# Kernel tuning notes

Hardware: AMD Instinct MI355X
Metric: run time of the kernel (lower is better)

Reference implementation:

```python
import jax, jax.numpy as jnp
import numpy as np

D_MODEL = 1024
D_HEAD = 128
B, S = 4, 4096


def apply_rope(x, cos, sin):
    # x: [B,S,d_head], cos/sin: [S, d_head//2]
    half = x.shape[-1] // 2
    x1, x2 = x[..., :half], x[..., half:]
    cos = cos[None, :, :].astype(x.dtype)
    sin = sin[None, :, :].astype(x.dtype)
    return jnp.concatenate([x1 * cos - x2 * sin, x1 * sin + x2 * cos], axis=-1)


def setup_inputs() -> dict:
    key = jax.random.key(0)
    ks = jax.random.split(key, 10)
    x = jax.random.normal(ks[0], (B, S, D_MODEL), dtype=jnp.float32)
    # realistic RoPE tables
    half = D_HEAD // 2
    inv_freq = 1.0 / (10000.0 ** (np.arange(0, half, dtype=np.float32) / half))
    pos = np.arange(S, dtype=np.float32)
    ang = pos[:, None] * inv_freq[None, :]
    cos = jnp.asarray(np.cos(ang), dtype=jnp.float32)
    sin = jnp.asarray(np.sin(ang), dtype=jnp.float32)
    # True where key index > query index (masked positions)
    causal_mask = jnp.triu(jnp.ones((S, S), dtype=bool), k=1)
    scale_w = 1.0 / np.sqrt(D_MODEL)
    Wq1 = jax.random.normal(ks[1], (D_MODEL, D_HEAD), dtype=jnp.float32) * scale_w
    Wq2 = jax.random.normal(ks[2], (D_MODEL, D_HEAD), dtype=jnp.float32) * scale_w
    Wk1 = jax.random.normal(ks[3], (D_MODEL, D_HEAD), dtype=jnp.float32) * scale_w
    Wk2 = jax.random.normal(ks[4], (D_MODEL, D_HEAD), dtype=jnp.float32) * scale_w
    Wv = jax.random.normal(ks[5], (D_MODEL, D_HEAD), dtype=jnp.float32) * scale_w
    Wo = jax.random.normal(ks[6], (D_HEAD, D_MODEL), dtype=jnp.float32) * (1.0 / np.sqrt(D_HEAD))
    return {"x": x, "cos": cos, "sin": sin, "causal_mask": causal_mask,
            "Wq1": Wq1, "Wq2": Wq2, "Wk1": Wk1, "Wk2": Wk2, "Wv": Wv, "Wo": Wo}


def reference(x, cos, sin, causal_mask, Wq1, Wq2, Wk1, Wk2, Wv, Wo):
    q1 = apply_rope(jnp.einsum('bsD,Dd->bsd', x, Wq1), cos, sin)
    q2 = apply_rope(jnp.einsum('bsD,Dd->bsd', x, Wq2), cos, sin)
    k1 = apply_rope(jnp.einsum('bsD,Dd->bsd', x, Wk1), cos, sin)
    k2 = apply_rope(jnp.einsum('bsD,Dd->bsd', x, Wk2), cos, sin)
    v = jnp.einsum('bsD,Dd->bsd', x, Wv)
    scale = 1.0 / np.sqrt(D_HEAD)
    a1 = jnp.einsum('bsd,btd->bst', q1, k1) * scale
    a2 = jnp.einsum('bsd,btd->bst', q2, k2) * scale
    a = jnp.where(causal_mask[None, :, :], 0.0, a1 * a2)
    out = jnp.einsum('bst,btd->bsd', a, v)
    return jnp.einsum('bsd,dD->bsD', out, Wo)
```

## Files before the change

kernel.cpp:

```cpp
#include <hip/hip_runtime.h>
#include <stdint.h>
#include <stddef.h>

typedef _Float16 f16;
typedef __attribute__((ext_vector_type(8))) _Float16 f16x8;
typedef __attribute__((ext_vector_type(4))) _Float16 f16x4;
typedef __attribute__((ext_vector_type(16))) float f32x16;
typedef __attribute__((ext_vector_type(8))) float f32x8v;
typedef __attribute__((ext_vector_type(4))) float floatx4;

#define MFMA(a, b, c) __builtin_amdgcn_mfma_f32_32x32x16_f16((a), (b), (c), 0, 0, 0)

typedef const __attribute__((address_space(1))) void gvoid_t;
typedef __attribute__((address_space(3))) void svoid_t;

__device__ __forceinline__ void gload_lds16(const void* g, void* l) {
  __builtin_amdgcn_global_load_lds((gvoid_t*)g, (svoid_t*)l, 16, 0, 0);
}

__global__ __launch_bounds__(256) void k_transpose_cvt(const float* __restrict__ W,
                                                       f16* __restrict__ Wt, int K, int N) {
  __shared__ float t[32][33];
  int k0 = blockIdx.x * 32, n0 = blockIdx.y * 32;
  int tx = threadIdx.x & 31, ty = threadIdx.x >> 5;
#pragma unroll
  for (int i = 0; i < 4; ++i)
    t[ty + 8 * i][tx] = W[(size_t)(k0 + ty + 8 * i) * N + n0 + tx];
  __syncthreads();
#pragma unroll
  for (int i = 0; i < 4; ++i)
    Wt[(size_t)(n0 + ty + 8 * i) * K + k0 + tx] = (f16)t[tx][ty + 8 * i];
}

__global__ __launch_bounds__(256, 2) void k_proj(const float* __restrict__ X,
                                                 const f16* __restrict__ Bt,
                                                 const float* __restrict__ cosp,
                                                 const float* __restrict__ sinp,
                                                 f16* __restrict__ q1h, f16* __restrict__ q2h,
                                                 f16* __restrict__ k1h, f16* __restrict__ k2h,
                                                 f16* __restrict__ vh) {
  __shared__ __align__(16) float Af[128 * 64];
  __shared__ __align__(16) f16 Bs[128 * 64];
  int tid = threadIdx.x;
  int wave = tid >> 6, lane = tid & 63;
  int m0 = blockIdx.y * 128, n0 = blockIdx.x;
  int wm = wave * 32;
  int rl = lane & 31, h = lane >> 5;
  int srow = lane >> 3, sslot = lane & 7;
  int arow = lane >> 4, aslot = lane & 15;
  const f16* Bmat = Bt + (size_t)n0 * 128 * 1024;

  f32x16 acc[4];
#pragma unroll
  for (int nb = 0; nb < 4; ++nb)
#pragma unroll
    for (int r = 0; r < 16; ++r) acc[nb][r] = 0.f;

  for (int k0 = 0; k0 < 1024; k0 += 64) {
    __syncthreads();
#pragma unroll
    for (int c = 0; c < 8; ++c) {
      int chunk = c * 4 + wave;
      int r = chunk * 4 + arow;
      int src16 = (((aslot >> 1) ^ (r & 7)) << 1) | (aslot & 1);
      gload_lds16(X + (size_t)(m0 + r) * 1024 + k0 + src16 * 4, Af + chunk * 256);
    }
#pragma unroll
    for (int c = 0; c < 4; ++c) {
      int chunk = c * 4 + wave;
      int r = chunk * 8 + srow;
      int cb = sslot ^ (r & 7);
      gload_lds16(Bmat + (size_t)r * 1024 + k0 + cb * 8, Bs + chunk * 512);
    }
    __syncthreads();

#pragma unroll
    for (int kb = 0; kb < 4; ++kb) {
      int s = 2 * kb + h;
      int ra = wm + rl;
      f32x8v a8 = *(const f32x8v*)(Af + ra * 64 + ((s ^ (ra & 7)) * 8));
      f16x8 af;
#pragma unroll
      for (int e = 0; e < 8; ++e) af[e] = (f16)a8[e];
      f16x8 bf[4];
#pragma unroll
      for (int nb = 0; nb < 4; ++nb) {
        int rb = nb * 32 + rl;
        bf[nb] = *(const f16x8*)(Bs + rb * 64 + (s ^ (rb & 7)) * 8);
      }
#pragma unroll
      for (int nb = 0; nb < 4; ++nb) acc[nb] = MFMA(af, bf[nb], acc[nb]);
    }
  }

  if (n0 == 4) {
#pragma unroll
    for (int r = 0; r < 16; ++r) {
      int irow = (r & 3) + 8 * (r >> 2) + 4 * h;
      int gr = m0 + wm + irow;
#pragma unroll
      for (int nb = 0; nb < 4; ++nb)
        vh[(size_t)gr * 128 + nb * 32 + rl] = (f16)acc[nb][r];
    }
  } else {
    f16* outp = (n0 == 0) ? q1h : (n0 == 1) ? q2h : (n0 == 2) ? k1h : k2h;
#pragma unroll
    for (int r = 0; r < 16; ++r) {
      int irow = (r & 3) + 8 * (r >> 2) + 4 * h;
      int gr = m0 + wm + irow;
      int s = gr & 4095;
#pragma unroll
      for (int nb = 0; nb < 2; ++nb) {
        int d = nb * 32 + rl;
        float c = cosp[s * 64 + d], sn = sinp[s * 64 + d];
        float a = acc[nb][r], bb = acc[nb + 2][r];
        outp[(size_t)gr * 128 + d]      = (f16)(a * c - bb * sn);
        outp[(size_t)gr * 128 + 64 + d] = (f16)(a * sn + bb * c);
      }
    }
  }
}

__global__ __launch_bounds__(256) void k_vtrans16(const f16* __restrict__ vh,
                                                  f16* __restrict__ vt) {
  __shared__ unsigned short t[32][33];
  int r0 = blockIdx.x * 32, d0 = blockIdx.y * 32;
  int tx = threadIdx.x & 31, ty = threadIdx.x >> 5;
#pragma unroll
  for (int i = 0; i < 4; ++i)
    t[ty + 8 * i][tx] = ((const unsigned short*)vh)[(size_t)(r0 + ty + 8 * i) * 128 + d0 + tx];
  __syncthreads();
  int b = r0 >> 12, s0 = r0 & 4095;
#pragma unroll
  for (int i = 0; i < 4; ++i)
    ((unsigned short*)vt)[((size_t)(b * 128 + d0 + ty + 8 * i)) * 4096 + s0 + tx] =
        t[tx][ty + 8 * i];
}

__global__ __launch_bounds__(256, 2) void k_s(const f16* __restrict__ q1h,
                                              const f16* __restrict__ q2h,
                                              const f16* __restrict__ k1h,
                                              const f16* __restrict__ k2h,
                                              f16* __restrict__ P) {
  __shared__ __align__(16) f16 A1[128 * 64];
  __shared__ __align__(16) f16 A2[128 * 64];
  __shared__ __align__(16) f16 B1[128 * 64];
  __shared__ __align__(16) f16 B2[128 * 64];
  int bid0 = blockIdx.x;
  int bid = (bid0 & 7) * 264 + (bid0 >> 3);
  int b = bid / 528, t = bid % 528;
  int i = (int)((sqrtf(8.f * t + 1.f) - 1.f) * 0.5f);
  if ((i + 1) * (i + 2) / 2 <= t) ++i;
  if (i * (i + 1) / 2 > t) --i;
  int j = t - i * (i + 1) / 2;

  int tid = threadIdx.x;
  int wave = tid >> 6, lane = tid & 63;
  int wm = (wave >> 1) * 64, wn = (wave & 1) * 64;
  int rl = lane & 31, h = lane >> 5;
  int srow = lane >> 3, sslot = lane & 7;
  size_t rowA = (size_t)b * 4096 + i * 128;
  size_t rowB = (size_t)b * 4096 + j * 128;

  f32x16 acc1[2][2], acc2[2][2];
#pragma unroll
  for (int mb = 0; mb < 2; ++mb)
#pragma unroll
    for (int nb = 0; nb < 2; ++nb)
#pragma unroll
      for (int r = 0; r < 16; ++r) { acc1[mb][nb][r] = 0.f; acc2[mb][nb][r] = 0.f; }

  for (int k0 = 0; k0 < 128; k0 += 64) {
    __syncthreads();
#pragma unroll
    for (int c = 0; c < 4; ++c) {
      int chunk = c * 4 + wave;
      int r = chunk * 8 + srow;
      int cb = sslot ^ (r & 7);
      gload_lds16(q1h + (rowA + r) * 128 + k0 + cb * 8, A1 + chunk * 512);
      gload_lds16(q2h + (rowA + r) * 128 + k0 + cb * 8, A2 + chunk * 512);
      gload_lds16(k1h + (rowB + r) * 128 + k0 + cb * 8, B1 + chunk * 512);
      gload_lds16(k2h + (rowB + r) * 128 + k0 + cb * 8, B2 + chunk * 512);
    }
    __syncthreads();

#pragma unroll
    for (int kb = 0; kb < 4; ++kb) {
      int s = 2 * kb + h;
      f16x8 a1f[2], a2f[2], b1f[2], b2f[2];
#pragma unroll
      for (int mb = 0; mb < 2; ++mb) {
        int r = wm + mb * 32 + rl;
        int off = r * 64 + (s ^ (r & 7)) * 8;
        a1f[mb] = *(const f16x8*)(A1 + off);
        a2f[mb] = *(const f16x8*)(A2 + off);
      }
#pragma unroll
      for (int nb = 0; nb < 2; ++nb) {
        int r = wn + nb * 32 + rl;
        int off = r * 64 + (s ^ (r & 7)) * 8;
        b1f[nb] = *(const f16x8*)(B1 + off);
        b2f[nb] = *(const f16x8*)(B2 + off);
      }
#pragma unroll
      for (int mb = 0; mb < 2; ++mb)
#pragma unroll
        for (int nb = 0; nb < 2; ++nb) {
          acc1[mb][nb] = MFMA(a1f[mb], b1f[nb], acc1[mb][nb]);
          acc2[mb][nb] = MFMA(a2f[mb], b2f[nb], acc2[mb][nb]);
        }
    }
  }

  f16* pt = P + ((size_t)b * 528 + t) * 16384;
  bool diag = (i == j);
#pragma unroll
  for (int mb = 0; mb < 2; ++mb)
#pragma unroll
    for (int nb = 0; nb < 2; ++nb)
#pragma unroll
      for (int r = 0; r < 16; ++r) {
        int row_l = wm + mb * 32 + (r & 3) + 8 * (r >> 2) + 4 * h;
        int col_l = wn + nb * 32 + rl;
        float p = acc1[mb][nb][r] * acc2[mb][nb][r] * (1.0f / 128.0f);
        if (diag && col_l > row_l) p = 0.f;
        pt[(size_t)row_l * 128 + col_l] = (f16)p;
      }
}

__global__ __launch_bounds__(256, 2) void k_pv(const f16* __restrict__ P,
                                               const f16* __restrict__ vt,
                                               f16* __restrict__ o0, f16* __restrict__ o1,
                                               f16* __restrict__ o2, f16* __restrict__ o3) {
  __shared__ __align__(16) f16 As[128 * 64];
  __shared__ __align__(16) f16 Bs[128 * 64];
  int bid = blockIdx.x;
  int b = bid / 80, c = bid % 80;
  int qt, s;
  if (c < 8)       { qt = c;                 s = 0; }
  else if (c < 24) { int t = c - 8;  qt = 8  + (t >> 1); s = t & 1; }
  else if (c < 48) { int t = c - 24; qt = 16 + t / 3;    s = t - 3 * (t / 3); }
  else             { int t = c - 48; qt = 24 + (t >> 2); s = t & 3; }
  int tq = qt * (qt + 1) / 2;
  const f16* Pb = P + (size_t)b * 528 * 16384;
  const f16* vb = vt + (size_t)b * 128 * 4096;
  int kbase = s * 1024;
  int kend = (qt + 1) * 128 < kbase + 1024 ? (qt + 1) * 128 : kbase + 1024;

  int tid = threadIdx.x;
  int wave = tid >> 6, lane = tid & 63;
  int wm = (wave >> 1) * 64, wn = (wave & 1) * 64;
  int rl = lane & 31, h = lane >> 5;
  int srow = lane >> 3, sslot = lane & 7;

  f32x16 acc[2][2];
#pragma unroll
  for (int mb = 0; mb < 2; ++mb)
#pragma unroll
    for (int nb = 0; nb < 2; ++nb)
#pragma unroll
      for (int r = 0; r < 16; ++r) acc[mb][nb][r] = 0.f;

  for (int k0 = kbase; k0 < kend; k0 += 64) {
    int jt = k0 >> 7, koff = k0 & 127;
    const f16* Pt = Pb + (size_t)(tq + jt) * 16384;
    __syncthreads();
#pragma unroll
    for (int c4 = 0; c4 < 4; ++c4) {
      int chunk = c4 * 4 + wave;
      int r = chunk * 8 + srow;
      int cb = sslot ^ (r & 7);
      gload_lds16(Pt + (size_t)r * 128 + koff + cb * 8, As + chunk * 512);
      gload_lds16(vb + (size_t)r * 4096 + k0 + cb * 8, Bs + chunk * 512);
    }
    __syncthreads();

#pragma unroll
    for (int kb = 0; kb < 4; ++kb) {
      int sidx = 2 * kb + h;
      f16x8 af[2], bf[2];
#pragma unroll
      for (int mb = 0; mb < 2; ++mb) {
        int r = wm + mb * 32 + rl;
        af[mb] = *(const f16x8*)(As + r * 64 + (sidx ^ (r & 7)) * 8);
      }
#pragma unroll
      for (int nb = 0; nb < 2; ++nb) {
        int r = wn + nb * 32 + rl;
        bf[nb] = *(const f16x8*)(Bs + r * 64 + (sidx ^ (r & 7)) * 8);
      }
#pragma unroll
      for (int mb = 0; mb < 2; ++mb)
#pragma unroll
        for (int nb = 0; nb < 2; ++nb)
          acc[mb][nb] = MFMA(af[mb], bf[nb], acc[mb][nb]);
    }
  }

  f16* op = (s == 0) ? o0 : (s == 1) ? o1 : (s == 2) ? o2 : o3;
#pragma unroll
  for (int mb = 0; mb < 2; ++mb)
#pragma unroll
    for (int nb = 0; nb < 2; ++nb)
#pragma unroll
      for (int r = 0; r < 16; ++r) {
        int gr = b * 4096 + qt * 128 + wm + mb * 32 + (r & 3) + 8 * (r >> 2) + 4 * h;
        op[(size_t)gr * 128 + wn + nb * 32 + rl] = (f16)acc[mb][nb][r];
      }
}

__global__ __launch_bounds__(256, 2) void k_gout(const f16* __restrict__ o0,
                                                 const f16* __restrict__ o1,
                                                 const f16* __restrict__ o2,
                                                 const f16* __restrict__ o3,
                                                 const f16* __restrict__ Bt,
                                                 float* __restrict__ C) {
  __shared__ __align__(16) f16 As[128 * 64];
  __shared__ __align__(16) f16 Bs[128 * 64];
  int tid = threadIdx.x;
  int wave = tid >> 6, lane = tid & 63;
  int m0 = blockIdx.y * 128, n0 = blockIdx.x * 128;
  int wm = (wave >> 1) * 64, wn = (wave & 1) * 64;
  int rl = lane & 31, h = lane >> 5;
  int srow = lane >> 3, sslot = lane & 7;
  int qt = (m0 >> 7) & 31;
  int ns = (qt >> 3) + 1;
  const f16* srcs[4] = {o0, o1, o2, o3};

  f32x16 acc[2][2];
#pragma unroll
  for (int mb = 0; mb < 2; ++mb)
#pragma unroll
    for (int nb = 0; nb < 2; ++nb)
#pragma unroll
      for (int r = 0; r < 16; ++r) acc[mb][nb][r] = 0.f;

  for (int k0 = 0; k0 < 128; k0 += 64) {
    __syncthreads();
#pragma unroll
    for (int c = 0; c < 4; ++c) {
      int chunk = c * 4 + wave;
      int r = chunk * 8 + srow;
      float sum[8];
#pragma unroll
      for (int e = 0; e < 8; ++e) sum[e] = 0.f;
#pragma unroll
      for (int p = 0; p < 4; ++p) {
        if (p < ns) {
          f16x8 v = *(const f16x8*)(srcs[p] + (size_t)(m0 + r) * 128 + k0 + sslot * 8);
#pragma unroll
          for (int e = 0; e < 8; ++e) sum[e] += (float)v[e];
        }
      }
      f16x8 w;
#pragma unroll
      for (int e = 0; e < 8; ++e) w[e] = (f16)sum[e];
      *(f16x8*)(As + r * 64 + (sslot ^ (r & 7)) * 8) = w;
      int cb = sslot ^ (r & 7);
      gload_lds16(Bt + (size_t)(n0 + r) * 128 + k0 + cb * 8, Bs + chunk * 512);
    }
    __syncthreads();

#pragma unroll
    for (int kb = 0; kb < 4; ++kb) {
      int s = 2 * kb + h;
      f16x8 af[2], bf[2];
#pragma unroll
      for (int mb = 0; mb < 2; ++mb) {
        int r = wm + mb * 32 + rl;
        af[mb] = *(const f16x8*)(As + r * 64 + (s ^ (r & 7)) * 8);
      }
#pragma unroll
      for (int nb = 0; nb < 2; ++nb) {
        int r = wn + nb * 32 + rl;
        bf[nb] = *(const f16x8*)(Bs + r * 64 + (s ^ (r & 7)) * 8);
      }
#pragma unroll
      for (int mb = 0; mb < 2; ++mb)
#pragma unroll
        for (int nb = 0; nb < 2; ++nb)
          acc[mb][nb] = MFMA(af[mb], bf[nb], acc[mb][nb]);
    }
  }

#pragma unroll
  for (int mb = 0; mb < 2; ++mb)
#pragma unroll
    for (int nb = 0; nb < 2; ++nb)
#pragma unroll
      for (int r = 0; r < 16; ++r) {
        int i = m0 + wm + mb * 32 + (r & 3) + 8 * (r >> 2) + 4 * h;
        int j = n0 + wn + nb * 32 + rl;
        C[(size_t)i * 1024 + j] = acc[mb][nb][r];
      }
}

extern "C" void kernel_launch(void* const* d_in, const int* in_sizes, int n_in,
                              void* d_out, int out_size, void* d_ws, size_t ws_size,
                              hipStream_t stream) {
  (void)in_sizes; (void)n_in; (void)out_size; (void)ws_size;
  const float* x  = (const float*)d_in[0];
  const float* cp = (const float*)d_in[1];
  const float* sp = (const float*)d_in[2];
  const float* W[5] = {(const float*)d_in[4], (const float*)d_in[5], (const float*)d_in[6],
                       (const float*)d_in[7], (const float*)d_in[8]};
  const float* Wo = (const float*)d_in[9];
  float* out = (float*)d_out;
  char* ws = (char*)d_ws;

  const size_t OFF_H    = 33554432;
  const size_t OFF_WTH  = OFF_H + 6 * 4194304;
  const size_t OFF_WOTH = OFF_WTH + 1310720;
  const size_t OFF_P    = OFF_WOTH + 262144;
  f16*   o0   = (f16*)(ws + 0);
  f16*   o1   = (f16*)(ws + 4194304);
  f16*   o2   = (f16*)(ws + 8388608);
  f16*   o3   = (f16*)(ws + 12582912);
  f16*   q1h  = (f16*)(ws + OFF_H + 0 * 4194304);
  f16*   q2h  = (f16*)(ws + OFF_H + 1 * 4194304);
  f16*   k1h  = (f16*)(ws + OFF_H + 2 * 4194304);
  f16*   k2h  = (f16*)(ws + OFF_H + 3 * 4194304);
  f16*   vh   = (f16*)(ws + OFF_H + 4 * 4194304);
  f16*   vt   = (f16*)(ws + OFF_H + 5 * 4194304);
  f16*   Wth  = (f16*)(ws + OFF_WTH);
  f16*   Woth = (f16*)(ws + OFF_WOTH);
  f16*   P    = (f16*)(ws + OFF_P);

  for (int w = 0; w < 5; ++w)
    k_transpose_cvt<<<dim3(32, 4), 256, 0, stream>>>(W[w], Wth + (size_t)w * 128 * 1024, 1024, 128);
  k_transpose_cvt<<<dim3(4, 32), 256, 0, stream>>>(Wo, Woth, 128, 1024);
  k_proj<<<dim3(5, 128), 256, 0, stream>>>(x, Wth, cp, sp, q1h, q2h, k1h, k2h, vh);
  k_vtrans16<<<dim3(512, 4), 256, 0, stream>>>(vh, vt);
  k_s<<<2112, 256, 0, stream>>>(q1h, q2h, k1h, k2h, P);
  k_pv<<<320, 256, 0, stream>>>(P, vt, o0, o1, o2, o3);
  k_gout<<<dim3(8, 128), 256, 0, stream>>>(o0, o1, o2, o3, Woth, out);
}
```

Measured before the change: 163.5 us.

## Pre-convert X to fp16 and remap projection block order for L2 locality

Result: faster. 151.4 us (-7.4%).

```diff
diff --git a/kernel.cpp b/kernel.cpp
--- a/kernel.cpp
+++ b/kernel.cpp
@@ -6,7 +6,6 @@
 typedef __attribute__((ext_vector_type(8))) _Float16 f16x8;
 typedef __attribute__((ext_vector_type(4))) _Float16 f16x4;
 typedef __attribute__((ext_vector_type(16))) float f32x16;
-typedef __attribute__((ext_vector_type(8))) float f32x8v;
 typedef __attribute__((ext_vector_type(4))) float floatx4;
 
 #define MFMA(a, b, c) __builtin_amdgcn_mfma_f32_32x32x16_f16((a), (b), (c), 0, 0, 0)
@@ -16,6 +15,17 @@
 
 __device__ __forceinline__ void gload_lds16(const void* g, void* l) {
   __builtin_amdgcn_global_load_lds((gvoid_t*)g, (svoid_t*)l, 16, 0, 0);
+}
+
+__global__ __launch_bounds__(256) void k_cvt_f16(const float* __restrict__ in,
+                                                 f16* __restrict__ out, int n4) {
+  int i = blockIdx.x * 256 + threadIdx.x;
+  if (i < n4) {
+    floatx4 v = ((const floatx4*)in)[i];
+    f16x4 o;
+    o[0] = (f16)v[0]; o[1] = (f16)v[1]; o[2] = (f16)v[2]; o[3] = (f16)v[3];
+    ((f16x4*)out)[i] = o;
+  }
 }
 
 __global__ __launch_bounds__(256) void k_transpose_cvt(const float* __restrict__ W,
@@ -32,22 +42,24 @@
     Wt[(size_t)(n0 + ty + 8 * i) * K + k0 + tx] = (f16)t[tx][ty + 8 * i];
 }
 
-__global__ __launch_bounds__(256, 2) void k_proj(const float* __restrict__ X,
+__global__ __launch_bounds__(256, 2) void k_proj(const f16* __restrict__ A,
                                                  const f16* __restrict__ Bt,
                                                  const float* __restrict__ cosp,
                                                  const float* __restrict__ sinp,
                                                  f16* __restrict__ q1h, f16* __restrict__ q2h,
                                                  f16* __restrict__ k1h, f16* __restrict__ k2h,
                                                  f16* __restrict__ vh) {
-  __shared__ __align__(16) float Af[128 * 64];
+  __shared__ __align__(16) f16 As[128 * 64];
   __shared__ __align__(16) f16 Bs[128 * 64];
+  int bid = blockIdx.x;
+  int c8 = bid & 7, t = bid >> 3;
+  int n0 = t % 5;
+  int m0 = (c8 + 8 * (t / 5)) * 128;
   int tid = threadIdx.x;
   int wave = tid >> 6, lane = tid & 63;
-  int m0 = blockIdx.y * 128, n0 = blockIdx.x;
   int wm = wave * 32;
   int rl = lane & 31, h = lane >> 5;
   int srow = lane >> 3, sslot = lane & 7;
-  int arow = lane >> 4, aslot = lane & 15;
   const f16* Bmat = Bt + (size_t)n0 * 128 * 1024;
 
   f32x16 acc[4];
@@ -58,18 +70,12 @@
 
   for (int k0 = 0; k0 < 1024; k0 += 64) {
     __syncthreads();
-#pragma unroll
-    for (int c = 0; c < 8; ++c) {
-      int chunk = c * 4 + wave;
-      int r = chunk * 4 + arow;
-      int src16 = (((aslot >> 1) ^ (r & 7)) << 1) | (aslot & 1);
-      gload_lds16(X + (size_t)(m0 + r) * 1024 + k0 + src16 * 4, Af + chunk * 256);
-    }
 #pragma unroll
     for (int c = 0; c < 4; ++c) {
       int chunk = c * 4 + wave;
       int r = chunk * 8 + srow;
       int cb = sslot ^ (r & 7);
+      gload_lds16(A + (size_t)(m0 + r) * 1024 + k0 + cb * 8, As + chunk * 512);
       gload_lds16(Bmat + (size_t)r * 1024 + k0 + cb * 8, Bs + chunk * 512);
     }
     __syncthreads();
@@ -78,10 +84,7 @@
     for (int kb = 0; kb < 4; ++kb) {
       int s = 2 * kb + h;
       int ra = wm + rl;
-      f32x8v a8 = *(const f32x8v*)(Af + ra * 64 + ((s ^ (ra & 7)) * 8));
-      f16x8 af;
-#pragma unroll
-      for (int e = 0; e < 8; ++e) af[e] = (f16)a8[e];
+      f16x8 af = *(const f16x8*)(As + ra * 64 + (s ^ (ra & 7)) * 8);
       f16x8 bf[4];
 #pragma unroll
       for (int nb = 0; nb < 4; ++nb) {
@@ -408,7 +411,8 @@
   float* out = (float*)d_out;
   char* ws = (char*)d_ws;
 
-  const size_t OFF_H    = 33554432;
+  const size_t OFF_XH   = 16777216;
+  const size_t OFF_H    = OFF_XH + 33554432;
   const size_t OFF_WTH  = OFF_H + 6 * 4194304;
   const size_t OFF_WOTH = OFF_WTH + 1310720;
   const size_t OFF_P    = OFF_WOTH + 262144;
@@ -416,6 +420,7 @@
   f16*   o1   = (f16*)(ws + 4194304);
   f16*   o2   = (f16*)(ws + 8388608);
   f16*   o3   = (f16*)(ws + 12582912);
+  f16*   xh   = (f16*)(ws + OFF_XH);
   f16*   q1h  = (f16*)(ws + OFF_H + 0 * 4194304);
   f16*   q2h  = (f16*)(ws + OFF_H + 1 * 4194304);
   f16*   k1h  = (f16*)(ws + OFF_H + 2 * 4194304);
@@ -426,10 +431,11 @@
   f16*   Woth = (f16*)(ws + OFF_WOTH);
   f16*   P    = (f16*)(ws + OFF_P);
 
+  k_cvt_f16<<<16384, 256, 0, stream>>>(x, xh, 4194304);
   for (int w = 0; w < 5; ++w)
     k_transpose_cvt<<<dim3(32, 4), 256, 0, stream>>>(W[w], Wth + (size_t)w * 128 * 1024, 1024, 128);
   k_transpose_cvt<<<dim3(4, 32), 256, 0, stream>>>(Wo, Woth, 128, 1024);
-  k_proj<<<dim3(5, 128), 256, 0, stream>>>(x, Wth, cp, sp, q1h, q2h, k1h, k2h, vh);
+  k_proj<<<640, 256, 0, stream>>>(xh, Wth, cp, sp, q1h, q2h, k1h, k2h, vh);
   k_vtrans16<<<dim3(512, 4), 256, 0, stream>>>(vh, vt);
   k_s<<<2112, 256, 0, stream>>>(q1h, q2h, k1h, k2h, P);
   k_pv<<<320, 256, 0, stream>>>(P, vt, o0, o1, o2, o3);
```
